# Kernel optimization log

Measured on AMD Instinct MI355X. Metric: run time of the kernel, lower is better.

Reference implementation:

```python
import jax, jax.numpy as jnp
import numpy as np

B, N, DIM, HEADS, DIM_HEAD = 2, 2048, 1024, 16, 64
INNER = HEADS * DIM_HEAD  # 1024
SCALE = DIM_HEAD ** -0.5
EPS = 1e-5  # fp32 path in the source


def _layernorm_seq(x, g):
    # Faithful to the repo's LayerNorm: statistics over dim=1 (sequence axis),
    # unbiased=False variance, clamp(min=eps).rsqrt(), scale by g over last axis.
    mean = jnp.mean(x, axis=1, keepdims=True)            # [b,1,d]
    var = jnp.mean((x - mean) ** 2, axis=1, keepdims=True)
    return (x - mean) * jax.lax.rsqrt(jnp.maximum(var, EPS)) * g


def setup_inputs() -> dict:
    key = jax.random.key(0)
    ks = jax.random.split(key, 5)
    x = jax.random.normal(ks[0], (B, N, DIM), dtype=jnp.float32)
    rel_pos_bias = jax.random.normal(ks[1], (1, HEADS, N, N), dtype=jnp.float32)
    g = jnp.ones((DIM,), dtype=jnp.float32)
    wq = jax.random.normal(ks[2], (INNER, DIM), dtype=jnp.float32) * (DIM ** -0.5)
    wkv = jax.random.normal(ks[3], (2 * INNER, DIM), dtype=jnp.float32) * (DIM ** -0.5)
    wout = jax.random.normal(ks[4], (DIM, INNER), dtype=jnp.float32) * (INNER ** -0.5)
    return {"x": x, "rel_pos_bias": rel_pos_bias, "g": g, "wq": wq, "wkv": wkv, "wout": wout}


def reference(x, rel_pos_bias, g, wq, wkv, wout):
    # self-attention path: context = x, framerate = None
    xn = _layernorm_seq(x, g)           # [b,n,d]
    cn = xn                              # context is None -> same tensor, same norm
    q = jnp.einsum('bnd,ed->bne', xn, wq)        # [b,n,inner]
    kv = jnp.einsum('bnd,ed->bne', cn, wkv)      # [b,n,2*inner]
    k, v = jnp.split(kv, 2, axis=-1)
    def heads(t):
        return t.reshape(B, N, HEADS, DIM_HEAD).transpose(0, 2, 1, 3)  # b h n d
    q, k, v = heads(q) * SCALE, heads(k), heads(v)
    sim = jnp.einsum('bhid,bhjd->bhij', q, k) + rel_pos_bias
    attn = jax.nn.softmax(sim, axis=-1)
    out = jnp.einsum('bhij,bhjd->bhid', attn, v)
    out = out.transpose(0, 2, 1, 3).reshape(B, N, INNER)  # b n (h d)
    return jnp.einsum('bne,de->bnd', out, wout)
```

## Files before the change

### kernel.cpp

```cpp
#include <hip/hip_runtime.h>
#include <hip/hip_bf16.h>
#include <stdint.h>

#define B_ 2
#define N_ 2048
#define DIM_ 1024
#define HEADS_ 16
#define DH_ 64
#define EPS_ 1e-5f

typedef __attribute__((ext_vector_type(4))) float f32x4;
typedef __attribute__((ext_vector_type(8))) float f32x8;
typedef __attribute__((ext_vector_type(16))) float f32x16;
typedef __attribute__((ext_vector_type(8))) __bf16 bf16x8;
typedef __attribute__((ext_vector_type(4))) unsigned int u32x4;
typedef __attribute__((ext_vector_type(2))) unsigned int u32x2;

__device__ __forceinline__ f32x4 mfma16(bf16x8 a, bf16x8 b, f32x4 c) {
  return __builtin_amdgcn_mfma_f32_16x16x32_bf16(a, b, c, 0, 0, 0);
}

__device__ __forceinline__ f32x16 mfma32(bf16x8 a, bf16x8 b, f32x16 c) {
  return __builtin_amdgcn_mfma_f32_32x32x16_bf16(a, b, c, 0, 0, 0);
}

__device__ __forceinline__ unsigned short f2bf(float x) {
  unsigned int u = __builtin_bit_cast(unsigned int, x);
  u += 0x7fffu + ((u >> 16) & 1u);
  return (unsigned short)(u >> 16);
}

__device__ __forceinline__ unsigned int cvt_pk_bf16(float lo, float hi) {
  unsigned int r;
  asm("v_cvt_pk_bf16_f32 %0, %1, %2" : "=v"(r) : "v"(lo), "v"(hi));
  return r;
}

__device__ __forceinline__ float uasf(unsigned int u) { return __builtin_bit_cast(float, u); }
__device__ __forceinline__ unsigned int fasu(float f) { return __builtin_bit_cast(unsigned int, f); }

__device__ __forceinline__ bf16x8 ld_frag(const unsigned short* p) {
  u32x4 v = *reinterpret_cast<const u32x4*>(p);
  return __builtin_bit_cast(bf16x8, v);
}

__device__ __forceinline__ void gload_lds16(const unsigned short* g, unsigned short* l) {
  __builtin_amdgcn_global_load_lds((const __attribute__((address_space(1))) void*)g,
                                   (__attribute__((address_space(3))) void*)l, 16, 0, 0);
}

__global__ __launch_bounds__(256) void ln_part(const float* __restrict__ x,
                                               float* __restrict__ ps,
                                               float* __restrict__ pss) {
  const int d = blockIdx.x * 256 + threadIdx.x;
  const int b = blockIdx.y >> 4, sp = blockIdx.y & 15;
  const float* xp = x + (size_t)(b * N_ + sp * 128) * DIM_ + d;
  float s = 0.f, ss = 0.f;
  for (int i = 0; i < 128; ++i) {
    float v = xp[(size_t)i * DIM_];
    s += v;
    ss += v * v;
  }
  int c = b * DIM_ + d;
  ps[sp * (B_ * DIM_) + c] = s;
  pss[sp * (B_ * DIM_) + c] = ss;
}

__global__ void ln_fin(const float* __restrict__ ps, const float* __restrict__ pss,
                       const float* __restrict__ g, float* __restrict__ meanA,
                       float* __restrict__ sclA) {
  int c = blockIdx.x * 256 + threadIdx.x;
  float s = 0.f, ss = 0.f;
#pragma unroll
  for (int sp = 0; sp < 16; ++sp) {
    s += ps[sp * (B_ * DIM_) + c];
    ss += pss[sp * (B_ * DIM_) + c];
  }
  float m = s * (1.f / N_);
  float v = ss * (1.f / N_) - m * m;
  meanA[c] = m;
  sclA[c] = rsqrtf(fmaxf(v, EPS_)) * g[c & (DIM_ - 1)];
}

__global__ __launch_bounds__(256) void ln_apply(const float* __restrict__ x,
                                                const float* __restrict__ meanA,
                                                const float* __restrict__ sclA,
                                                unsigned short* __restrict__ xn) {
  size_t t = (size_t)blockIdx.x * 256 + threadIdx.x;
  size_t base = t * 8;
  int d0 = (int)(base & (DIM_ - 1));
  int b = base >= (size_t)N_ * DIM_;
  int c = b * DIM_ + d0;
  const float4* xp = reinterpret_cast<const float4*>(x + base);
  const float4* mp = reinterpret_cast<const float4*>(meanA + c);
  const float4* sp = reinterpret_cast<const float4*>(sclA + c);
  float4 x0 = xp[0], x1 = xp[1];
  float4 m0 = mp[0], m1 = mp[1];
  float4 s0 = sp[0], s1 = sp[1];
  union {
    unsigned short u[8];
    u32x4 v;
  } o;
  o.u[0] = f2bf((x0.x - m0.x) * s0.x);
  o.u[1] = f2bf((x0.y - m0.y) * s0.y);
  o.u[2] = f2bf((x0.z - m0.z) * s0.z);
  o.u[3] = f2bf((x0.w - m0.w) * s0.w);
  o.u[4] = f2bf((x1.x - m1.x) * s1.x);
  o.u[5] = f2bf((x1.y - m1.y) * s1.y);
  o.u[6] = f2bf((x1.z - m1.z) * s1.z);
  o.u[7] = f2bf((x1.w - m1.w) * s1.w);
  *reinterpret_cast<u32x4*>(xn + base) = o.v;
}

__global__ __launch_bounds__(256) void cast_bf16(const float* __restrict__ src,
                                                 unsigned short* __restrict__ dst, float scale) {
  size_t t = (size_t)blockIdx.x * 256 + threadIdx.x;
  size_t base = t * 8;
  const float4* sp = reinterpret_cast<const float4*>(src + base);
  float4 a = sp[0], b4 = sp[1];
  union {
    unsigned short u[8];
    u32x4 v;
  } o;
  o.u[0] = f2bf(a.x * scale);
  o.u[1] = f2bf(a.y * scale);
  o.u[2] = f2bf(a.z * scale);
  o.u[3] = f2bf(a.w * scale);
  o.u[4] = f2bf(b4.x * scale);
  o.u[5] = f2bf(b4.y * scale);
  o.u[6] = f2bf(b4.z * scale);
  o.u[7] = f2bf(b4.w * scale);
  *reinterpret_cast<u32x4*>(dst + base) = o.v;
}

template <bool OUT_F32>
__global__ __launch_bounds__(256) void gemm_bt(const unsigned short* __restrict__ A,
                                               const unsigned short* __restrict__ W,
                                               void* __restrict__ Cout, int K, int ldc) {
  __shared__ unsigned short sA[128 * 64];
  __shared__ unsigned short sB[128 * 64];
  const int tid = threadIdx.x, lane = tid & 63, w = tid >> 6;
  const int wm = w >> 1, wn = w & 1;
  const int l15 = lane & 15, l4 = lane >> 4;
  const int m0 = blockIdx.y * 128, n0 = blockIdx.x * 128;
  f32x4 acc[4][4] = {};
  for (int kt = 0; kt < K; kt += 64) {
    __syncthreads();
#pragma unroll
    for (int p = 0; p < 4; ++p) {
      int flat = p * 256 + tid;
      int row = flat >> 3, c = flat & 7;
      int cs = c ^ (row & 7);
      gload_lds16(A + (size_t)(m0 + row) * K + kt + cs * 8, sA + (size_t)(p * 256 + w * 64) * 8);
      gload_lds16(W + (size_t)(n0 + row) * K + kt + cs * 8, sB + (size_t)(p * 256 + w * 64) * 8);
    }
    __syncthreads();
#pragma unroll
    for (int kk = 0; kk < 2; ++kk) {
      bf16x8 af[4], bfr[4];
#pragma unroll
      for (int i = 0; i < 4; ++i) {
        int rowA = wm * 64 + i * 16 + l15;
        af[i] = ld_frag(sA + rowA * 64 + (((kk * 4 + l4) ^ (rowA & 7)) * 8));
        int rowB = wn * 64 + i * 16 + l15;
        bfr[i] = ld_frag(sB + rowB * 64 + (((kk * 4 + l4) ^ (rowB & 7)) * 8));
      }
#pragma unroll
      for (int i = 0; i < 4; ++i)
#pragma unroll
        for (int j = 0; j < 4; ++j) acc[i][j] = mfma16(af[i], bfr[j], acc[i][j]);
    }
  }
#pragma unroll
  for (int i = 0; i < 4; ++i)
#pragma unroll
    for (int j = 0; j < 4; ++j)
#pragma unroll
      for (int r = 0; r < 4; ++r) {
        size_t off =
            (size_t)(m0 + wm * 64 + i * 16 + l4 * 4 + r) * ldc + (n0 + wn * 64 + j * 16 + l15);
        if (OUT_F32)
          ((float*)Cout)[off] = acc[i][j][r];
        else
          ((unsigned short*)Cout)[off] = f2bf(acc[i][j][r]);
      }
}

__global__ __launch_bounds__(256) void transpose_v(const unsigned short* __restrict__ qkv,
                                                   unsigned short* __restrict__ Vt) {
  __shared__ unsigned short tt[64][65];
  const int tid = threadIdx.x;
  const int h = blockIdx.y >> 1, b = blockIdx.y & 1;
  const int n0 = blockIdx.x * 64;
  const unsigned short* src = qkv + (size_t)(b * N_ + n0) * 3072 + 2048 + h * 64;
#pragma unroll
  for (int i = 0; i < 16; ++i) {
    int idx = i * 256 + tid;
    int r = idx >> 6, c = idx & 63;
    tt[r][c] = src[(size_t)r * 3072 + c];
  }
  __syncthreads();
  unsigned short* dst = Vt + (size_t)(b * HEADS_ + h) * 64 * N_ + n0;
#pragma unroll
  for (int i = 0; i < 16; ++i) {
    int idx = i * 256 + tid;
    int dh = idx >> 6, nn = idx & 63;
    dst[(size_t)dh * N_ + nn] = tt[nn][dh];
  }
}

__global__ __launch_bounds__(512, 2) void flash_attn(const unsigned short* __restrict__ qkv,
                                                     const float* __restrict__ bias,
                                                     const unsigned short* __restrict__ Vt,
                                                     unsigned short* __restrict__ Oatt) {
  __shared__ unsigned short sK[128 * 64];
  __shared__ unsigned short sV[64 * 128];
  __shared__ float sBias[8][32 * 128];

  const int tid = threadIdx.x, lane = tid & 63, w = tid >> 6;
  const int l31 = lane & 31, hi = lane >> 5;
  const int r = blockIdx.x;
  const int bh = r & 31, iblk = r >> 5;
  const int h = bh & 15, b = bh >> 4;
  const int qbase = iblk * 256 + w * 32;

  const unsigned short* Kg = qkv + (size_t)b * N_ * 3072 + 1024 + h * 64;
  const unsigned short* VtB = Vt + (size_t)(b * HEADS_ + h) * 64 * N_;
  const float* bias_h = bias + (size_t)h * N_ * N_;

  const int kflat0 = tid, kflat1 = 512 + tid;
  const int krow0 = kflat0 >> 3, kc0 = (kflat0 & 7) ^ (krow0 & 7);
  const int krow1 = kflat1 >> 3, kc1 = (kflat1 & 7) ^ (krow1 & 7);
  const int vrow0 = kflat0 >> 4, vc0 = (kflat0 & 15) ^ (vrow0 & 15);
  const int vrow1 = kflat1 >> 4, vc1 = (kflat1 & 15) ^ (vrow1 & 15);
  unsigned short* sKb0 = sK + (size_t)(w * 64) * 8;
  unsigned short* sKb1 = sK + (size_t)(512 + w * 64) * 8;
  unsigned short* sVb0 = sV + (size_t)(w * 64) * 8;
  unsigned short* sVb1 = sV + (size_t)(512 + w * 64) * 8;

#define STAGE_KV(JN)                                                       \
  gload_lds16(Kg + (size_t)((JN) + krow0) * 3072 + kc0 * 8, sKb0);         \
  gload_lds16(Kg + (size_t)((JN) + krow1) * 3072 + kc1 * 8, sKb1);         \
  gload_lds16(VtB + (size_t)vrow0 * N_ + (JN) + vc0 * 8, sVb0);            \
  gload_lds16(VtB + (size_t)vrow1 * N_ + (JN) + vc1 * 8, sVb1);

  float* sBw = sBias[w];
  unsigned short* sBw_us = reinterpret_cast<unsigned short*>(sBw);
  const int brr = lane >> 5, bsl = lane & 31;
  const float* bQ = bias_h + (size_t)qbase * N_;
#define SBI(i, JN)                                                            \
  gload_lds16((const unsigned short*)(bQ + (size_t)(2 * (i) + brr) * N_ +     \
                                      (JN) + ((bsl ^ (2 * (i) + brr)) << 2)), \
              sBw_us + (i) * 512);
#define STAGE_BIAS(JN)                                                     \
  SBI(0, JN) SBI(1, JN) SBI(2, JN) SBI(3, JN) SBI(4, JN) SBI(5, JN)        \
  SBI(6, JN) SBI(7, JN) SBI(8, JN) SBI(9, JN) SBI(10, JN) SBI(11, JN)      \
  SBI(12, JN) SBI(13, JN) SBI(14, JN) SBI(15, JN)

#define LDBIAS(DST, CB)                                                        \
  {                                                                            \
    const float* myB_ = sBw + l31 * 128;                                       \
    f32x4 t0 = *reinterpret_cast<const f32x4*>(myB_ + ((((CB) + 0 + hi) ^ l31) << 2)); \
    f32x4 t1 = *reinterpret_cast<const f32x4*>(myB_ + ((((CB) + 2 + hi) ^ l31) << 2)); \
    f32x4 t2 = *reinterpret_cast<const f32x4*>(myB_ + ((((CB) + 4 + hi) ^ l31) << 2)); \
    f32x4 t3 = *reinterpret_cast<const f32x4*>(myB_ + ((((CB) + 6 + hi) ^ l31) << 2)); \
    f32x8 u0_ = __builtin_shufflevector(t0, t1, 0, 1, 2, 3, 4, 5, 6, 7);       \
    f32x8 u1_ = __builtin_shufflevector(t2, t3, 0, 1, 2, 3, 4, 5, 6, 7);       \
    DST = __builtin_shufflevector(u0_, u1_, 0, 1, 2, 3, 4, 5, 6, 7, 8, 9, 10,  \
                                  11, 12, 13, 14, 15);                         \
  }

#define FRAGK(OUT, ROWB, CH)                                              \
  {                                                                       \
    int row_ = (ROWB) + l31;                                              \
    OUT = ld_frag(sK + row_ * 64 + (((CH) ^ (row_ & 7)) * 8));            \
  }
#define FRAGV(OUT, ROWB, CH)                                              \
  {                                                                       \
    int row_ = (ROWB) + l31;                                              \
    OUT = ld_frag(sV + row_ * 128 + (((CH) ^ (row_ & 15)) * 8));          \
  }

#define PACK2(S, PLO, PHI)                                                 \
  {                                                                        \
    unsigned int w0 = cvt_pk_bf16(S[0], S[1]), w1 = cvt_pk_bf16(S[2], S[3]);     \
    unsigned int w2 = cvt_pk_bf16(S[4], S[5]), w3 = cvt_pk_bf16(S[6], S[7]);     \
    unsigned int w4 = cvt_pk_bf16(S[8], S[9]), w5 = cvt_pk_bf16(S[10], S[11]);   \
    unsigned int w6 = cvt_pk_bf16(S[12], S[13]), w7 = cvt_pk_bf16(S[14], S[15]); \
    auto rA = __builtin_amdgcn_permlane32_swap(w0, w2, false, false);      \
    auto rB = __builtin_amdgcn_permlane32_swap(w1, w3, false, false);      \
    auto rC = __builtin_amdgcn_permlane32_swap(w4, w6, false, false);      \
    auto rD = __builtin_amdgcn_permlane32_swap(w5, w7, false, false);      \
    u32x4 pw;                                                              \
    pw[0] = rA[0]; pw[1] = rB[0]; pw[2] = rA[1]; pw[3] = rB[1];            \
    PLO = __builtin_bit_cast(bf16x8, pw);                                  \
    pw[0] = rC[0]; pw[1] = rD[0]; pw[2] = rC[1]; pw[3] = rD[1];            \
    PHI = __builtin_bit_cast(bf16x8, pw);                                  \
  }

  bf16x8 qf0, qf1, qf2, qf3;
  {
    const unsigned short* Qg =
        qkv + (size_t)(b * N_ + qbase + l31) * 3072 + h * 64 + hi * 8;
    qf0 = ld_frag(Qg);
    qf1 = ld_frag(Qg + 16);
    qf2 = ld_frag(Qg + 32);
    qf3 = ld_frag(Qg + 48);
  }

  f32x16 o0 = {}, o1 = {};
  float m_run = -1e30f, l_run = 0.f;

  STAGE_KV(0)
  STAGE_BIAS(0)

  const int NP = N_ / 128;
  for (int p = 0; p < NP; ++p) {
    asm volatile("s_waitcnt vmcnt(0) lgkmcnt(0)" ::: "memory");
    __builtin_amdgcn_s_barrier();

    f32x16 SA0, SA1, SB0, SB1;
    LDBIAS(SA0, 0)
    LDBIAS(SA1, 8)
    LDBIAS(SB0, 16)
    LDBIAS(SB1, 24)
    asm volatile("s_waitcnt lgkmcnt(0)" ::: "memory");
    __builtin_amdgcn_sched_barrier(0);

    if (p + 1 < NP) {
      const size_t jn = (size_t)(p + 1) * 128;
      STAGE_BIAS(jn)
    }

    __builtin_amdgcn_s_setprio(1);
    {
      bf16x8 kf;
      FRAGK(kf, 0, 0 + hi)  SA0 = mfma32(kf, qf0, SA0);
      FRAGK(kf, 0, 2 + hi)  SA0 = mfma32(kf, qf1, SA0);
      FRAGK(kf, 0, 4 + hi)  SA0 = mfma32(kf, qf2, SA0);
      FRAGK(kf, 0, 6 + hi)  SA0 = mfma32(kf, qf3, SA0);
      FRAGK(kf, 32, 0 + hi) SA1 = mfma32(kf, qf0, SA1);
      FRAGK(kf, 32, 2 + hi) SA1 = mfma32(kf, qf1, SA1);
      FRAGK(kf, 32, 4 + hi) SA1 = mfma32(kf, qf2, SA1);
      FRAGK(kf, 32, 6 + hi) SA1 = mfma32(kf, qf3, SA1);
      FRAGK(kf, 64, 0 + hi) SB0 = mfma32(kf, qf0, SB0);
      FRAGK(kf, 64, 2 + hi) SB0 = mfma32(kf, qf1, SB0);
      FRAGK(kf, 64, 4 + hi) SB0 = mfma32(kf, qf2, SB0);
      FRAGK(kf, 64, 6 + hi) SB0 = mfma32(kf, qf3, SB0);
      FRAGK(kf, 96, 0 + hi) SB1 = mfma32(kf, qf0, SB1);
      FRAGK(kf, 96, 2 + hi) SB1 = mfma32(kf, qf1, SB1);
      FRAGK(kf, 96, 4 + hi) SB1 = mfma32(kf, qf2, SB1);
      FRAGK(kf, 96, 6 + hi) SB1 = mfma32(kf, qf3, SB1);
    }
    __builtin_amdgcn_s_setprio(0);

    float c0 = SA0[0], c1 = SA1[0], c2 = SB0[0], c3 = SB1[0];
#pragma unroll
    for (int i = 1; i < 16; ++i) {
      c0 = fmaxf(c0, SA0[i]);
      c1 = fmaxf(c1, SA1[i]);
      c2 = fmaxf(c2, SB0[i]);
      c3 = fmaxf(c3, SB1[i]);
    }
    float mx = fmaxf(fmaxf(c0, c1), fmaxf(c2, c3));
    {
      auto pr_ = __builtin_amdgcn_permlane32_swap(fasu(mx), fasu(mx), false, false);
      mx = fmaxf(uasf(pr_[0]), uasf(pr_[1]));
    }
    float mn = fmaxf(m_run, mx);
    float alpha = __expf(m_run - mn);
#pragma unroll
    for (int i = 0; i < 16; ++i) {
      SA0[i] = __expf(SA0[i] - mn);
      SA1[i] = __expf(SA1[i] - mn);
      SB0[i] = __expf(SB0[i] - mn);
      SB1[i] = __expf(SB1[i] - mn);
    }
    float r0 = 0.f, r1 = 0.f, r2 = 0.f, r3 = 0.f;
#pragma unroll
    for (int i = 0; i < 16; ++i) {
      r0 += SA0[i];
      r1 += SA1[i];
      r2 += SB0[i];
      r3 += SB1[i];
    }
    float rs = (r0 + r1) + (r2 + r3);
    {
      auto pr_ = __builtin_amdgcn_permlane32_swap(fasu(rs), fasu(rs), false, false);
      rs = uasf(pr_[0]) + uasf(pr_[1]);
    }
    l_run = l_run * alpha + rs;
    m_run = mn;
#pragma unroll
    for (int i = 0; i < 16; ++i) {
      o0[i] *= alpha;
      o1[i] *= alpha;
    }

    bf16x8 pA0, pA1, pA2, pA3, pB0, pB1, pB2, pB3;
    PACK2(SA0, pA0, pA1)
    PACK2(SA1, pA2, pA3)
    PACK2(SB0, pB0, pB1)
    PACK2(SB1, pB2, pB3)

    __builtin_amdgcn_s_setprio(1);
    {
      bf16x8 vf;
      FRAGV(vf, 0, 0 + hi)   o0 = mfma32(vf, pA0, o0);
      FRAGV(vf, 0, 2 + hi)   o0 = mfma32(vf, pA1, o0);
      FRAGV(vf, 0, 4 + hi)   o0 = mfma32(vf, pA2, o0);
      FRAGV(vf, 0, 6 + hi)   o0 = mfma32(vf, pA3, o0);
      FRAGV(vf, 0, 8 + hi)   o0 = mfma32(vf, pB0, o0);
      FRAGV(vf, 0, 10 + hi)  o0 = mfma32(vf, pB1, o0);
      FRAGV(vf, 0, 12 + hi)  o0 = mfma32(vf, pB2, o0);
      FRAGV(vf, 0, 14 + hi)  o0 = mfma32(vf, pB3, o0);
      FRAGV(vf, 32, 0 + hi)  o1 = mfma32(vf, pA0, o1);
      FRAGV(vf, 32, 2 + hi)  o1 = mfma32(vf, pA1, o1);
      FRAGV(vf, 32, 4 + hi)  o1 = mfma32(vf, pA2, o1);
      FRAGV(vf, 32, 6 + hi)  o1 = mfma32(vf, pA3, o1);
      FRAGV(vf, 32, 8 + hi)  o1 = mfma32(vf, pB0, o1);
      FRAGV(vf, 32, 10 + hi) o1 = mfma32(vf, pB1, o1);
      FRAGV(vf, 32, 12 + hi) o1 = mfma32(vf, pB2, o1);
      FRAGV(vf, 32, 14 + hi) o1 = mfma32(vf, pB3, o1);
    }
    __builtin_amdgcn_s_setprio(0);

    asm volatile("s_waitcnt lgkmcnt(0)" ::: "memory");
    __builtin_amdgcn_s_barrier();
    if (p + 1 < NP) {
      const size_t jn = (size_t)(p + 1) * 128;
      STAGE_KV(jn)
    }
  }
#undef STAGE_KV
#undef SBI
#undef STAGE_BIAS
#undef LDBIAS
#undef FRAGK
#undef FRAGV
#undef PACK2

  float inv = 1.f / l_run;
  unsigned short* orow =
      Oatt + (size_t)(b * N_ + qbase + l31) * 1024 + h * 64 + hi * 4;
#pragma unroll
  for (int g = 0; g < 4; ++g) {
    u32x2 pk0;
    pk0[0] = cvt_pk_bf16(o0[g * 4 + 0] * inv, o0[g * 4 + 1] * inv);
    pk0[1] = cvt_pk_bf16(o0[g * 4 + 2] * inv, o0[g * 4 + 3] * inv);
    *reinterpret_cast<u32x2*>(orow + g * 8) = pk0;
    u32x2 pk1;
    pk1[0] = cvt_pk_bf16(o1[g * 4 + 0] * inv, o1[g * 4 + 1] * inv);
    pk1[1] = cvt_pk_bf16(o1[g * 4 + 2] * inv, o1[g * 4 + 3] * inv);
    *reinterpret_cast<u32x2*>(orow + 32 + g * 8) = pk1;
  }
}

extern "C" void kernel_launch(void* const* d_in, const int* in_sizes, int n_in, void* d_out,
                              int out_size, void* d_ws, size_t ws_size, hipStream_t stream) {
  const float* x = (const float*)d_in[0];
  const float* bias = (const float*)d_in[1];
  const float* g = (const float*)d_in[2];
  const float* wq = (const float*)d_in[3];
  const float* wkv = (const float*)d_in[4];
  const float* wout = (const float*)d_in[5];
  float* out = (float*)d_out;

  float* ps = (float*)d_ws;
  float* pss = ps + 16 * B_ * DIM_;
  float* meanA = pss + 16 * B_ * DIM_;
  float* sclA = meanA + B_ * DIM_;
  unsigned short* xn = (unsigned short*)(sclA + B_ * DIM_);
  unsigned short* Wqkv = xn + (size_t)4096 * 1024;
  unsigned short* WoutB = Wqkv + (size_t)3072 * 1024;
  unsigned short* qkvb = WoutB + (size_t)1024 * 1024;
  unsigned short* Vt = qkvb + (size_t)4096 * 3072;
  unsigned short* Oatt = xn;

  ln_part<<<dim3(DIM_ / 256, B_ * 16), 256, 0, stream>>>(x, ps, pss);
  ln_fin<<<dim3((B_ * DIM_) / 256), 256, 0, stream>>>(ps, pss, g, meanA, sclA);
  ln_apply<<<dim3((B_ * N_ * DIM_) / 2048), 256, 0, stream>>>(x, meanA, sclA, xn);
  cast_bf16<<<dim3((DIM_ * DIM_) / 2048), 256, 0, stream>>>(wq, Wqkv, 0.125f);
  cast_bf16<<<dim3((2 * DIM_ * DIM_) / 2048), 256, 0, stream>>>(wkv, Wqkv + (size_t)DIM_ * DIM_,
                                                                1.0f);
  cast_bf16<<<dim3((DIM_ * DIM_) / 2048), 256, 0, stream>>>(wout, WoutB, 1.0f);
  gemm_bt<false><<<dim3(3072 / 128, 4096 / 128), 256, 0, stream>>>(xn, Wqkv, qkvb, DIM_, 3072);
  transpose_v<<<dim3(N_ / 64, B_ * HEADS_), 256, 0, stream>>>(qkvb, Vt);
  flash_attn<<<dim3(256), 512, 0, stream>>>(qkvb, bias, Vt, Oatt);
  gemm_bt<true><<<dim3(1024 / 128, 4096 / 128), 256, 0, stream>>>(Oatt, WoutB, out, DIM_, 1024);
}
```

Baseline: 173.8 us.

## Double-buffer K/V and bias tiles with 64-key steps in flash attention

Shrinks the key tile from 128 to 64 and double-buffers the K, V and bias shared-memory tiles. Loads for the next K/V tile and the bias tile two steps ahead are issued while the current tile is computed, with a partial vmcnt wait in place of a full drain. This also removes the second barrier per iteration. In exchange the loop runs twice as many iterations, each with its own softmax rescale and barrier, and the swizzle and wait-count logic is more intricate.

```diff
diff --git a/kernel.cpp b/kernel.cpp
--- a/kernel.cpp
+++ b/kernel.cpp
@@ -213,72 +213,67 @@
                                                      const float* __restrict__ bias,
                                                      const unsigned short* __restrict__ Vt,
                                                      unsigned short* __restrict__ Oatt) {
-  __shared__ unsigned short sK[128 * 64];
-  __shared__ unsigned short sV[64 * 128];
-  __shared__ float sBias[8][32 * 128];
+  __shared__ unsigned short sK[2][64 * 64];
+  __shared__ unsigned short sV[2][64 * 64];
+  __shared__ float sBias[8][2][32 * 64];
 
   const int tid = threadIdx.x, lane = tid & 63, w = tid >> 6;
   const int l31 = lane & 31, hi = lane >> 5;
   const int r = blockIdx.x;
   const int bh = r & 31, iblk = r >> 5;
   const int h = bh & 15, b = bh >> 4;
-  const int qbase = iblk * 256 + w * 32;
+  const int qwb = iblk * 256 + w * 32;
 
   const unsigned short* Kg = qkv + (size_t)b * N_ * 3072 + 1024 + h * 64;
   const unsigned short* VtB = Vt + (size_t)(b * HEADS_ + h) * 64 * N_;
   const float* bias_h = bias + (size_t)h * N_ * N_;
 
-  const int kflat0 = tid, kflat1 = 512 + tid;
-  const int krow0 = kflat0 >> 3, kc0 = (kflat0 & 7) ^ (krow0 & 7);
-  const int krow1 = kflat1 >> 3, kc1 = (kflat1 & 7) ^ (krow1 & 7);
-  const int vrow0 = kflat0 >> 4, vc0 = (kflat0 & 15) ^ (vrow0 & 15);
-  const int vrow1 = kflat1 >> 4, vc1 = (kflat1 & 15) ^ (vrow1 & 15);
-  unsigned short* sKb0 = sK + (size_t)(w * 64) * 8;
-  unsigned short* sKb1 = sK + (size_t)(512 + w * 64) * 8;
-  unsigned short* sVb0 = sV + (size_t)(w * 64) * 8;
-  unsigned short* sVb1 = sV + (size_t)(512 + w * 64) * 8;
-
-#define STAGE_KV(JN)                                                       \
-  gload_lds16(Kg + (size_t)((JN) + krow0) * 3072 + kc0 * 8, sKb0);         \
-  gload_lds16(Kg + (size_t)((JN) + krow1) * 3072 + kc1 * 8, sKb1);         \
-  gload_lds16(VtB + (size_t)vrow0 * N_ + (JN) + vc0 * 8, sVb0);            \
-  gload_lds16(VtB + (size_t)vrow1 * N_ + (JN) + vc1 * 8, sVb1);
-
-  float* sBw = sBias[w];
-  unsigned short* sBw_us = reinterpret_cast<unsigned short*>(sBw);
-  const int brr = lane >> 5, bsl = lane & 31;
-  const float* bQ = bias_h + (size_t)qbase * N_;
-#define SBI(i, JN)                                                            \
-  gload_lds16((const unsigned short*)(bQ + (size_t)(2 * (i) + brr) * N_ +     \
-                                      (JN) + ((bsl ^ (2 * (i) + brr)) << 2)), \
-              sBw_us + (i) * 512);
-#define STAGE_BIAS(JN)                                                     \
-  SBI(0, JN) SBI(1, JN) SBI(2, JN) SBI(3, JN) SBI(4, JN) SBI(5, JN)        \
-  SBI(6, JN) SBI(7, JN) SBI(8, JN) SBI(9, JN) SBI(10, JN) SBI(11, JN)      \
-  SBI(12, JN) SBI(13, JN) SBI(14, JN) SBI(15, JN)
-
-#define LDBIAS(DST, CB)                                                        \
+  const int krow = w * 8 + (lane >> 3);
+  const int kcs = (lane & 7) ^ (krow & 7);
+  const unsigned short* kSrc = Kg + (size_t)krow * 3072 + kcs * 8;
+  const unsigned short* vSrc = VtB + (size_t)krow * N_ + kcs * 8;
+
+#define STAGE_KV(S, JN)                                      \
+  gload_lds16(kSrc + (size_t)(JN) * 3072, sK[S] + w * 512);  \
+  gload_lds16(vSrc + (JN), sV[S] + w * 512);
+
+  const int ln4b = lane >> 4, l15b = lane & 15;
+  const float* bp0 =
+      bias_h + (size_t)(qwb + 0 + ln4b) * N_ + ((l15b ^ ((0 + ln4b) & 15)) << 2);
+  const float* bp1 =
+      bias_h + (size_t)(qwb + 4 + ln4b) * N_ + ((l15b ^ ((4 + ln4b) & 15)) << 2);
+  const float* bp2 =
+      bias_h + (size_t)(qwb + 8 + ln4b) * N_ + ((l15b ^ ((8 + ln4b) & 15)) << 2);
+  const float* bp3 =
+      bias_h + (size_t)(qwb + 12 + ln4b) * N_ + ((l15b ^ ((12 + ln4b) & 15)) << 2);
+
+#define STAGE_BIAS(DSTUS, JN)                                                  \
+  gload_lds16((const unsigned short*)(bp0 + (JN)), (DSTUS) + 0 * 512);         \
+  gload_lds16((const unsigned short*)(bp1 + (JN)), (DSTUS) + 1 * 512);         \
+  gload_lds16((const unsigned short*)(bp2 + (JN)), (DSTUS) + 2 * 512);         \
+  gload_lds16((const unsigned short*)(bp3 + (JN)), (DSTUS) + 3 * 512);         \
+  gload_lds16((const unsigned short*)(bp0 + 16 * N_ + (JN)), (DSTUS) + 4 * 512); \
+  gload_lds16((const unsigned short*)(bp1 + 16 * N_ + (JN)), (DSTUS) + 5 * 512); \
+  gload_lds16((const unsigned short*)(bp2 + 16 * N_ + (JN)), (DSTUS) + 6 * 512); \
+  gload_lds16((const unsigned short*)(bp3 + 16 * N_ + (JN)), (DSTUS) + 7 * 512);
+
+#define LDBIAS(DST, MYB, CHB)                                                  \
   {                                                                            \
-    const float* myB_ = sBw + l31 * 128;                                       \
-    f32x4 t0 = *reinterpret_cast<const f32x4*>(myB_ + ((((CB) + 0 + hi) ^ l31) << 2)); \
-    f32x4 t1 = *reinterpret_cast<const f32x4*>(myB_ + ((((CB) + 2 + hi) ^ l31) << 2)); \
-    f32x4 t2 = *reinterpret_cast<const f32x4*>(myB_ + ((((CB) + 4 + hi) ^ l31) << 2)); \
-    f32x4 t3 = *reinterpret_cast<const f32x4*>(myB_ + ((((CB) + 6 + hi) ^ l31) << 2)); \
+    const float* myB_ = (MYB) + (size_t)l31 * 64;                              \
+    f32x4 t0 = *reinterpret_cast<const f32x4*>(myB_ + ((((CHB) + 0 + hi) ^ (l31 & 15)) << 2)); \
+    f32x4 t1 = *reinterpret_cast<const f32x4*>(myB_ + ((((CHB) + 2 + hi) ^ (l31 & 15)) << 2)); \
+    f32x4 t2 = *reinterpret_cast<const f32x4*>(myB_ + ((((CHB) + 4 + hi) ^ (l31 & 15)) << 2)); \
+    f32x4 t3 = *reinterpret_cast<const f32x4*>(myB_ + ((((CHB) + 6 + hi) ^ (l31 & 15)) << 2)); \
     f32x8 u0_ = __builtin_shufflevector(t0, t1, 0, 1, 2, 3, 4, 5, 6, 7);       \
     f32x8 u1_ = __builtin_shufflevector(t2, t3, 0, 1, 2, 3, 4, 5, 6, 7);       \
     DST = __builtin_shufflevector(u0_, u1_, 0, 1, 2, 3, 4, 5, 6, 7, 8, 9, 10,  \
                                   11, 12, 13, 14, 15);                         \
   }
 
-#define FRAGK(OUT, ROWB, CH)                                              \
-  {                                                                       \
-    int row_ = (ROWB) + l31;                                              \
-    OUT = ld_frag(sK + row_ * 64 + (((CH) ^ (row_ & 7)) * 8));            \
-  }
-#define FRAGV(OUT, ROWB, CH)                                              \
-  {                                                                       \
-    int row_ = (ROWB) + l31;                                              \
-    OUT = ld_frag(sV + row_ * 128 + (((CH) ^ (row_ & 15)) * 8));          \
+#define FRAGK(OUT, SRC, ROWB, CH)                                       \
+  {                                                                     \
+    int row_ = (ROWB) + l31;                                            \
+    OUT = ld_frag((SRC) + row_ * 64 + (((CH) ^ (row_ & 7)) * 8));       \
   }
 
 #define PACK2(S, PLO, PHI)                                                 \
@@ -301,7 +296,7 @@
   bf16x8 qf0, qf1, qf2, qf3;
   {
     const unsigned short* Qg =
-        qkv + (size_t)(b * N_ + qbase + l31) * 3072 + h * 64 + hi * 8;
+        qkv + (size_t)(b * N_ + qwb + l31) * 3072 + h * 64 + hi * 8;
     qf0 = ld_frag(Qg);
     qf1 = ld_frag(Qg + 16);
     qf2 = ld_frag(Qg + 32);
@@ -311,58 +306,62 @@
   f32x16 o0 = {}, o1 = {};
   float m_run = -1e30f, l_run = 0.f;
 
-  STAGE_KV(0)
-  STAGE_BIAS(0)
-
-  const int NP = N_ / 128;
-  for (int p = 0; p < NP; ++p) {
-    asm volatile("s_waitcnt vmcnt(0) lgkmcnt(0)" ::: "memory");
+  STAGE_BIAS(reinterpret_cast<unsigned short*>(&sBias[w][0][0]), 0)
+  __builtin_amdgcn_sched_barrier(0);
+  STAGE_KV(0, 0)
+  __builtin_amdgcn_sched_barrier(0);
+  STAGE_BIAS(reinterpret_cast<unsigned short*>(&sBias[w][1][0]), 64)
+  __builtin_amdgcn_sched_barrier(0);
+
+  const int NT = N_ / 64;
+  for (int j = 0; j < NT; ++j) {
+    if (j == NT - 1)
+      asm volatile("s_waitcnt vmcnt(0)" ::: "memory");
+    else
+      asm volatile("s_waitcnt vmcnt(8)" ::: "memory");
     __builtin_amdgcn_s_barrier();
-
-    f32x16 SA0, SA1, SB0, SB1;
-    LDBIAS(SA0, 0)
-    LDBIAS(SA1, 8)
-    LDBIAS(SB0, 16)
-    LDBIAS(SB1, 24)
+    const int slot = j & 1;
+    const unsigned short* sKc = sK[slot];
+    const unsigned short* sVc = sV[slot];
+    float* sBw = &sBias[w][slot][0];
+
+    if (j + 1 < NT) {
+      STAGE_KV(slot ^ 1, (size_t)(j + 1) * 64)
+      __builtin_amdgcn_sched_barrier(0);
+    }
+
+    f32x16 SA0, SA1;
+    LDBIAS(SA0, sBw, 0)
+    LDBIAS(SA1, sBw, 8)
     asm volatile("s_waitcnt lgkmcnt(0)" ::: "memory");
     __builtin_amdgcn_sched_barrier(0);
 
-    if (p + 1 < NP) {
-      const size_t jn = (size_t)(p + 1) * 128;
-      STAGE_BIAS(jn)
+    if (j + 2 < NT) {
+      STAGE_BIAS(reinterpret_cast<unsigned short*>(sBw), (size_t)(j + 2) * 64)
+      __builtin_amdgcn_sched_barrier(0);
     }
 
     __builtin_amdgcn_s_setprio(1);
     {
       bf16x8 kf;
-      FRAGK(kf, 0, 0 + hi)  SA0 = mfma32(kf, qf0, SA0);
-      FRAGK(kf, 0, 2 + hi)  SA0 = mfma32(kf, qf1, SA0);
-      FRAGK(kf, 0, 4 + hi)  SA0 = mfma32(kf, qf2, SA0);
-      FRAGK(kf, 0, 6 + hi)  SA0 = mfma32(kf, qf3, SA0);
-      FRAGK(kf, 32, 0 + hi) SA1 = mfma32(kf, qf0, SA1);
-      FRAGK(kf, 32, 2 + hi) SA1 = mfma32(kf, qf1, SA1);
-      FRAGK(kf, 32, 4 + hi) SA1 = mfma32(kf, qf2, SA1);
-      FRAGK(kf, 32, 6 + hi) SA1 = mfma32(kf, qf3, SA1);
-      FRAGK(kf, 64, 0 + hi) SB0 = mfma32(kf, qf0, SB0);
-      FRAGK(kf, 64, 2 + hi) SB0 = mfma32(kf, qf1, SB0);
-      FRAGK(kf, 64, 4 + hi) SB0 = mfma32(kf, qf2, SB0);
-      FRAGK(kf, 64, 6 + hi) SB0 = mfma32(kf, qf3, SB0);
-      FRAGK(kf, 96, 0 + hi) SB1 = mfma32(kf, qf0, SB1);
-      FRAGK(kf, 96, 2 + hi) SB1 = mfma32(kf, qf1, SB1);
-      FRAGK(kf, 96, 4 + hi) SB1 = mfma32(kf, qf2, SB1);
-      FRAGK(kf, 96, 6 + hi) SB1 = mfma32(kf, qf3, SB1);
+      FRAGK(kf, sKc, 0, 0 + hi)  SA0 = mfma32(kf, qf0, SA0);
+      FRAGK(kf, sKc, 0, 2 + hi)  SA0 = mfma32(kf, qf1, SA0);
+      FRAGK(kf, sKc, 0, 4 + hi)  SA0 = mfma32(kf, qf2, SA0);
+      FRAGK(kf, sKc, 0, 6 + hi)  SA0 = mfma32(kf, qf3, SA0);
+      FRAGK(kf, sKc, 32, 0 + hi) SA1 = mfma32(kf, qf0, SA1);
+      FRAGK(kf, sKc, 32, 2 + hi) SA1 = mfma32(kf, qf1, SA1);
+      FRAGK(kf, sKc, 32, 4 + hi) SA1 = mfma32(kf, qf2, SA1);
+      FRAGK(kf, sKc, 32, 6 + hi) SA1 = mfma32(kf, qf3, SA1);
     }
     __builtin_amdgcn_s_setprio(0);
 
-    float c0 = SA0[0], c1 = SA1[0], c2 = SB0[0], c3 = SB1[0];
+    float c0 = SA0[0], c1 = SA1[0];
 #pragma unroll
     for (int i = 1; i < 16; ++i) {
       c0 = fmaxf(c0, SA0[i]);
       c1 = fmaxf(c1, SA1[i]);
-      c2 = fmaxf(c2, SB0[i]);
-      c3 = fmaxf(c3, SB1[i]);
-    }
-    float mx = fmaxf(fmaxf(c0, c1), fmaxf(c2, c3));
+    }
+    float mx = fmaxf(c0, c1);
     {
       auto pr_ = __builtin_amdgcn_permlane32_swap(fasu(mx), fasu(mx), false, false);
       mx = fmaxf(uasf(pr_[0]), uasf(pr_[1]));
@@ -373,18 +372,14 @@
     for (int i = 0; i < 16; ++i) {
       SA0[i] = __expf(SA0[i] - mn);
       SA1[i] = __expf(SA1[i] - mn);
-      SB0[i] = __expf(SB0[i] - mn);
-      SB1[i] = __expf(SB1[i] - mn);
-    }
-    float r0 = 0.f, r1 = 0.f, r2 = 0.f, r3 = 0.f;
+    }
+    float r0 = 0.f, r1 = 0.f;
 #pragma unroll
     for (int i = 0; i < 16; ++i) {
       r0 += SA0[i];
       r1 += SA1[i];
-      r2 += SB0[i];
-      r3 += SB1[i];
-    }
-    float rs = (r0 + r1) + (r2 + r3);
+    }
+    float rs = r0 + r1;
     {
       auto pr_ = __builtin_amdgcn_permlane32_swap(fasu(rs), fasu(rs), false, false);
       rs = uasf(pr_[0]) + uasf(pr_[1]);
@@ -397,52 +392,33 @@
       o1[i] *= alpha;
     }
 
-    bf16x8 pA0, pA1, pA2, pA3, pB0, pB1, pB2, pB3;
+    bf16x8 pA0, pA1, pA2, pA3;
     PACK2(SA0, pA0, pA1)
     PACK2(SA1, pA2, pA3)
-    PACK2(SB0, pB0, pB1)
-    PACK2(SB1, pB2, pB3)
 
     __builtin_amdgcn_s_setprio(1);
     {
       bf16x8 vf;
-      FRAGV(vf, 0, 0 + hi)   o0 = mfma32(vf, pA0, o0);
-      FRAGV(vf, 0, 2 + hi)   o0 = mfma32(vf, pA1, o0);
-      FRAGV(vf, 0, 4 + hi)   o0 = mfma32(vf, pA2, o0);
-      FRAGV(vf, 0, 6 + hi)   o0 = mfma32(vf, pA3, o0);
-      FRAGV(vf, 0, 8 + hi)   o0 = mfma32(vf, pB0, o0);
-      FRAGV(vf, 0, 10 + hi)  o0 = mfma32(vf, pB1, o0);
-      FRAGV(vf, 0, 12 + hi)  o0 = mfma32(vf, pB2, o0);
-      FRAGV(vf, 0, 14 + hi)  o0 = mfma32(vf, pB3, o0);
-      FRAGV(vf, 32, 0 + hi)  o1 = mfma32(vf, pA0, o1);
-      FRAGV(vf, 32, 2 + hi)  o1 = mfma32(vf, pA1, o1);
-      FRAGV(vf, 32, 4 + hi)  o1 = mfma32(vf, pA2, o1);
-      FRAGV(vf, 32, 6 + hi)  o1 = mfma32(vf, pA3, o1);
-      FRAGV(vf, 32, 8 + hi)  o1 = mfma32(vf, pB0, o1);
-      FRAGV(vf, 32, 10 + hi) o1 = mfma32(vf, pB1, o1);
-      FRAGV(vf, 32, 12 + hi) o1 = mfma32(vf, pB2, o1);
-      FRAGV(vf, 32, 14 + hi) o1 = mfma32(vf, pB3, o1);
+      FRAGK(vf, sVc, 0, 0 + hi)  o0 = mfma32(vf, pA0, o0);
+      FRAGK(vf, sVc, 0, 2 + hi)  o0 = mfma32(vf, pA1, o0);
+      FRAGK(vf, sVc, 0, 4 + hi)  o0 = mfma32(vf, pA2, o0);
+      FRAGK(vf, sVc, 0, 6 + hi)  o0 = mfma32(vf, pA3, o0);
+      FRAGK(vf, sVc, 32, 0 + hi) o1 = mfma32(vf, pA0, o1);
+      FRAGK(vf, sVc, 32, 2 + hi) o1 = mfma32(vf, pA1, o1);
+      FRAGK(vf, sVc, 32, 4 + hi) o1 = mfma32(vf, pA2, o1);
+      FRAGK(vf, sVc, 32, 6 + hi) o1 = mfma32(vf, pA3, o1);
     }
     __builtin_amdgcn_s_setprio(0);
-
-    asm volatile("s_waitcnt lgkmcnt(0)" ::: "memory");
-    __builtin_amdgcn_s_barrier();
-    if (p + 1 < NP) {
-      const size_t jn = (size_t)(p + 1) * 128;
-      STAGE_KV(jn)
-    }
   }
 #undef STAGE_KV
-#undef SBI
 #undef STAGE_BIAS
 #undef LDBIAS
 #undef FRAGK
-#undef FRAGV
 #undef PACK2
 
   float inv = 1.f / l_run;
   unsigned short* orow =
-      Oatt + (size_t)(b * N_ + qbase + l31) * 1024 + h * 64 + hi * 4;
+      Oatt + (size_t)(b * N_ + qwb + l31) * 1024 + h * 64 + hi * 4;
 #pragma unroll
   for (int g = 0; g < 4; ++g) {
     u32x2 pk0;
```

Result: slower. 189.3 us (+8.9%).

## Share relative-position bias tiles across both batches in flash attention blocks

Applied to the files above, without the earlier changes.

Each workgroup now covers one head and 128 query rows for both batch elements. Waves 0-3 take batch 0 and waves 4-7 take batch 1 over the same query rows, so the bias tile (which has no batch dimension) is loaded into LDS once and used by both halves. This halves global bias traffic, which is the dominant stream here. In exchange, K/V LDS buffers double to hold both batches, every wave stages part of the shared bias, and an extra barrier is added after reading bias so it is not overwritten by the next prefetch.

```diff
diff --git a/kernel.cpp b/kernel.cpp
--- a/kernel.cpp
+++ b/kernel.cpp
@@ -213,53 +213,89 @@
                                                      const float* __restrict__ bias,
                                                      const unsigned short* __restrict__ Vt,
                                                      unsigned short* __restrict__ Oatt) {
-  __shared__ unsigned short sK[128 * 64];
-  __shared__ unsigned short sV[64 * 128];
-  __shared__ float sBias[8][32 * 128];
+  __shared__ unsigned short sK[2 * 128 * 64];
+  __shared__ unsigned short sV[2 * 64 * 128];
+  __shared__ float sBias[4][32 * 128];
 
   const int tid = threadIdx.x, lane = tid & 63, w = tid >> 6;
   const int l31 = lane & 31, hi = lane >> 5;
-  const int r = blockIdx.x;
-  const int bh = r & 31, iblk = r >> 5;
-  const int h = bh & 15, b = bh >> 4;
-  const int qbase = iblk * 256 + w * 32;
-
-  const unsigned short* Kg = qkv + (size_t)b * N_ * 3072 + 1024 + h * 64;
-  const unsigned short* VtB = Vt + (size_t)(b * HEADS_ + h) * 64 * N_;
+  const int id = blockIdx.x;
+  const int h = id & 15, iblk = id >> 4;
+  const int sl = w & 3, wb = w >> 2;
+  const int qwb = iblk * 128 + sl * 32;
+
+  const unsigned short* Kg0 = qkv + 1024 + h * 64;
+  const unsigned short* Kg1 = Kg0 + (size_t)N_ * 3072;
+  const unsigned short* Vt0 = Vt + (size_t)h * 64 * N_;
+  const unsigned short* Vt1 = Vt0 + (size_t)HEADS_ * 64 * N_;
   const float* bias_h = bias + (size_t)h * N_ * N_;
 
-  const int kflat0 = tid, kflat1 = 512 + tid;
-  const int krow0 = kflat0 >> 3, kc0 = (kflat0 & 7) ^ (krow0 & 7);
-  const int krow1 = kflat1 >> 3, kc1 = (kflat1 & 7) ^ (krow1 & 7);
-  const int vrow0 = kflat0 >> 4, vc0 = (kflat0 & 15) ^ (vrow0 & 15);
-  const int vrow1 = kflat1 >> 4, vc1 = (kflat1 & 15) ^ (vrow1 & 15);
-  unsigned short* sKb0 = sK + (size_t)(w * 64) * 8;
-  unsigned short* sKb1 = sK + (size_t)(512 + w * 64) * 8;
-  unsigned short* sVb0 = sV + (size_t)(w * 64) * 8;
-  unsigned short* sVb1 = sV + (size_t)(512 + w * 64) * 8;
-
-#define STAGE_KV(JN)                                                       \
-  gload_lds16(Kg + (size_t)((JN) + krow0) * 3072 + kc0 * 8, sKb0);         \
-  gload_lds16(Kg + (size_t)((JN) + krow1) * 3072 + kc1 * 8, sKb1);         \
-  gload_lds16(VtB + (size_t)vrow0 * N_ + (JN) + vc0 * 8, sVb0);            \
-  gload_lds16(VtB + (size_t)vrow1 * N_ + (JN) + vc1 * 8, sVb1);
-
-  float* sBw = sBias[w];
-  unsigned short* sBw_us = reinterpret_cast<unsigned short*>(sBw);
+  const int krow_t = tid >> 3, kcs_t = (tid & 7) ^ (krow_t & 7);
+  const unsigned short* kS0 = Kg0 + (size_t)krow_t * 3072 + kcs_t * 8;
+  const unsigned short* kS1 = kS0 + (size_t)64 * 3072;
+  const unsigned short* kS2 = Kg1 + (size_t)krow_t * 3072 + kcs_t * 8;
+  const unsigned short* kS3 = kS2 + (size_t)64 * 3072;
+  unsigned short* kD0 = sK + (size_t)(0 * 512 + w * 64) * 8;
+  unsigned short* kD1 = sK + (size_t)(1 * 512 + w * 64) * 8;
+  unsigned short* kD2 = sK + (size_t)(2 * 512 + w * 64) * 8;
+  unsigned short* kD3 = sK + (size_t)(3 * 512 + w * 64) * 8;
+
+  const int vrow_t = tid >> 4, vcs_t = (tid & 15) ^ (vrow_t & 15);
+  const unsigned short* vS0 = Vt0 + (size_t)vrow_t * N_ + vcs_t * 8;
+  const unsigned short* vS1 = vS0 + (size_t)32 * N_;
+  const unsigned short* vS2 = Vt1 + (size_t)vrow_t * N_ + vcs_t * 8;
+  const unsigned short* vS3 = vS2 + (size_t)32 * N_;
+  unsigned short* vD0 = sV + (size_t)(0 * 512 + w * 64) * 8;
+  unsigned short* vD1 = sV + (size_t)(1 * 512 + w * 64) * 8;
+  unsigned short* vD2 = sV + (size_t)(2 * 512 + w * 64) * 8;
+  unsigned short* vD3 = sV + (size_t)(3 * 512 + w * 64) * 8;
+
+#define STAGE_KV(JN)                                  \
+  gload_lds16(kS0 + (size_t)(JN) * 3072, kD0);        \
+  gload_lds16(kS1 + (size_t)(JN) * 3072, kD1);        \
+  gload_lds16(kS2 + (size_t)(JN) * 3072, kD2);        \
+  gload_lds16(kS3 + (size_t)(JN) * 3072, kD3);        \
+  gload_lds16(vS0 + (JN), vD0);                       \
+  gload_lds16(vS1 + (JN), vD1);                       \
+  gload_lds16(vS2 + (JN), vD2);                       \
+  gload_lds16(vS3 + (JN), vD3);
+
   const int brr = lane >> 5, bsl = lane & 31;
-  const float* bQ = bias_h + (size_t)qbase * N_;
-#define SBI(i, JN)                                                            \
-  gload_lds16((const unsigned short*)(bQ + (size_t)(2 * (i) + brr) * N_ +     \
-                                      (JN) + ((bsl ^ (2 * (i) + brr)) << 2)), \
-              sBw_us + (i) * 512);
-#define STAGE_BIAS(JN)                                                     \
-  SBI(0, JN) SBI(1, JN) SBI(2, JN) SBI(3, JN) SBI(4, JN) SBI(5, JN)        \
-  SBI(6, JN) SBI(7, JN) SBI(8, JN) SBI(9, JN) SBI(10, JN) SBI(11, JN)      \
-  SBI(12, JN) SBI(13, JN) SBI(14, JN) SBI(15, JN)
+  const int rl0 = 16 * wb + 0 + brr, rl1 = 16 * wb + 2 + brr;
+  const int rl2 = 16 * wb + 4 + brr, rl3 = 16 * wb + 6 + brr;
+  const int rl4 = 16 * wb + 8 + brr, rl5 = 16 * wb + 10 + brr;
+  const int rl6 = 16 * wb + 12 + brr, rl7 = 16 * wb + 14 + brr;
+  const float* bq0 = bias_h + (size_t)(qwb + rl0) * N_ + ((bsl ^ rl0) << 2);
+  const float* bq1 = bias_h + (size_t)(qwb + rl1) * N_ + ((bsl ^ rl1) << 2);
+  const float* bq2 = bias_h + (size_t)(qwb + rl2) * N_ + ((bsl ^ rl2) << 2);
+  const float* bq3 = bias_h + (size_t)(qwb + rl3) * N_ + ((bsl ^ rl3) << 2);
+  const float* bq4 = bias_h + (size_t)(qwb + rl4) * N_ + ((bsl ^ rl4) << 2);
+  const float* bq5 = bias_h + (size_t)(qwb + rl5) * N_ + ((bsl ^ rl5) << 2);
+  const float* bq6 = bias_h + (size_t)(qwb + rl6) * N_ + ((bsl ^ rl6) << 2);
+  const float* bq7 = bias_h + (size_t)(qwb + rl7) * N_ + ((bsl ^ rl7) << 2);
+  unsigned short* sB_us = reinterpret_cast<unsigned short*>(sBias[sl]);
+  unsigned short* bD0 = sB_us + (size_t)(16 * wb + 0) * 256;
+  unsigned short* bD1 = sB_us + (size_t)(16 * wb + 2) * 256;
+  unsigned short* bD2 = sB_us + (size_t)(16 * wb + 4) * 256;
+  unsigned short* bD3 = sB_us + (size_t)(16 * wb + 6) * 256;
+  unsigned short* bD4 = sB_us + (size_t)(16 * wb + 8) * 256;
+  unsigned short* bD5 = sB_us + (size_t)(16 * wb + 10) * 256;
+  unsigned short* bD6 = sB_us + (size_t)(16 * wb + 12) * 256;
+  unsigned short* bD7 = sB_us + (size_t)(16 * wb + 14) * 256;
+
+#define STAGE_BIAS(JN)                                        \
+  gload_lds16((const unsigned short*)(bq0 + (JN)), bD0);      \
+  gload_lds16((const unsigned short*)(bq1 + (JN)), bD1);      \
+  gload_lds16((const unsigned short*)(bq2 + (JN)), bD2);      \
+  gload_lds16((const unsigned short*)(bq3 + (JN)), bD3);      \
+  gload_lds16((const unsigned short*)(bq4 + (JN)), bD4);      \
+  gload_lds16((const unsigned short*)(bq5 + (JN)), bD5);      \
+  gload_lds16((const unsigned short*)(bq6 + (JN)), bD6);      \
+  gload_lds16((const unsigned short*)(bq7 + (JN)), bD7);
 
 #define LDBIAS(DST, CB)                                                        \
   {                                                                            \
-    const float* myB_ = sBw + l31 * 128;                                       \
+    const float* myB_ = sBias[sl] + (size_t)l31 * 128;                         \
     f32x4 t0 = *reinterpret_cast<const f32x4*>(myB_ + ((((CB) + 0 + hi) ^ l31) << 2)); \
     f32x4 t1 = *reinterpret_cast<const f32x4*>(myB_ + ((((CB) + 2 + hi) ^ l31) << 2)); \
     f32x4 t2 = *reinterpret_cast<const f32x4*>(myB_ + ((((CB) + 4 + hi) ^ l31) << 2)); \
@@ -270,15 +306,18 @@
                                   11, 12, 13, 14, 15);                         \
   }
 
-#define FRAGK(OUT, ROWB, CH)                                              \
-  {                                                                       \
-    int row_ = (ROWB) + l31;                                              \
-    OUT = ld_frag(sK + row_ * 64 + (((CH) ^ (row_ & 7)) * 8));            \
-  }
-#define FRAGV(OUT, ROWB, CH)                                              \
-  {                                                                       \
-    int row_ = (ROWB) + l31;                                              \
-    OUT = ld_frag(sV + row_ * 128 + (((CH) ^ (row_ & 15)) * 8));          \
+  const unsigned short* sKb = sK + (size_t)wb * 128 * 64;
+  const unsigned short* sVb = sV + (size_t)wb * 64 * 128;
+
+#define FRAGK(OUT, ROWB, CH)                                            \
+  {                                                                     \
+    int row_ = (ROWB) + l31;                                            \
+    OUT = ld_frag(sKb + row_ * 64 + (((CH) ^ (row_ & 7)) * 8));         \
+  }
+#define FRAGV(OUT, ROWB, CH)                                            \
+  {                                                                     \
+    int row_ = (ROWB) + l31;                                            \
+    OUT = ld_frag(sVb + row_ * 128 + (((CH) ^ (row_ & 15)) * 8));       \
   }
 
 #define PACK2(S, PLO, PHI)                                                 \
@@ -301,7 +340,7 @@
   bf16x8 qf0, qf1, qf2, qf3;
   {
     const unsigned short* Qg =
-        qkv + (size_t)(b * N_ + qbase + l31) * 3072 + h * 64 + hi * 8;
+        qkv + (size_t)(wb * N_ + qwb + l31) * 3072 + h * 64 + hi * 8;
     qf0 = ld_frag(Qg);
     qf1 = ld_frag(Qg + 16);
     qf2 = ld_frag(Qg + 32);
@@ -326,6 +365,7 @@
     LDBIAS(SB1, 24)
     asm volatile("s_waitcnt lgkmcnt(0)" ::: "memory");
     __builtin_amdgcn_sched_barrier(0);
+    __builtin_amdgcn_s_barrier();
 
     if (p + 1 < NP) {
       const size_t jn = (size_t)(p + 1) * 128;
@@ -433,7 +473,6 @@
     }
   }
 #undef STAGE_KV
-#undef SBI
 #undef STAGE_BIAS
 #undef LDBIAS
 #undef FRAGK
@@ -442,7 +481,7 @@
 
   float inv = 1.f / l_run;
   unsigned short* orow =
-      Oatt + (size_t)(b * N_ + qbase + l31) * 1024 + h * 64 + hi * 4;
+      Oatt + (size_t)(wb * N_ + qwb + l31) * 1024 + h * 64 + hi * 4;
 #pragma unroll
   for (int g = 0; g < 4; ++g) {
     u32x2 pk0;
```

New measurement: 174.4 us. Within noise of the previous version (+0.4%).

## Double-buffer bias tiles and shrink attention blocks to four waves

Applied to the files above, without the earlier changes.

The flash attention kernel now runs 512 blocks of 256 threads (4 waves, 128 query rows) instead of 256 blocks of 512 threads. The bias tile in LDS is double-buffered per wave, so the next tile's bias loads are issued before the current tile's compute and waited on with a partial vmcnt instead of a full drain. The goal is to hide the large fp32 bias stream behind the MFMA work and to spread work over more blocks. In exchange, LDS per block grows, K/V tiles are reloaded by twice as many blocks, and occupancy is limited by launch bounds of one block.

```diff
diff --git a/kernel.cpp b/kernel.cpp
--- a/kernel.cpp
+++ b/kernel.cpp
@@ -209,57 +209,57 @@
   }
 }
 
-__global__ __launch_bounds__(512, 2) void flash_attn(const unsigned short* __restrict__ qkv,
+__global__ __launch_bounds__(256, 1) void flash_attn(const unsigned short* __restrict__ qkv,
                                                      const float* __restrict__ bias,
                                                      const unsigned short* __restrict__ Vt,
                                                      unsigned short* __restrict__ Oatt) {
   __shared__ unsigned short sK[128 * 64];
   __shared__ unsigned short sV[64 * 128];
-  __shared__ float sBias[8][32 * 128];
+  __shared__ float sBias[4][2][32 * 128];
 
   const int tid = threadIdx.x, lane = tid & 63, w = tid >> 6;
   const int l31 = lane & 31, hi = lane >> 5;
-  const int r = blockIdx.x;
-  const int bh = r & 31, iblk = r >> 5;
+  const int id = blockIdx.x;
+  const int bh = id & 31, iblk = id >> 5;
   const int h = bh & 15, b = bh >> 4;
-  const int qbase = iblk * 256 + w * 32;
+  const int qwb = iblk * 128 + w * 32;
 
   const unsigned short* Kg = qkv + (size_t)b * N_ * 3072 + 1024 + h * 64;
   const unsigned short* VtB = Vt + (size_t)(b * HEADS_ + h) * 64 * N_;
   const float* bias_h = bias + (size_t)h * N_ * N_;
 
-  const int kflat0 = tid, kflat1 = 512 + tid;
-  const int krow0 = kflat0 >> 3, kc0 = (kflat0 & 7) ^ (krow0 & 7);
-  const int krow1 = kflat1 >> 3, kc1 = (kflat1 & 7) ^ (krow1 & 7);
-  const int vrow0 = kflat0 >> 4, vc0 = (kflat0 & 15) ^ (vrow0 & 15);
-  const int vrow1 = kflat1 >> 4, vc1 = (kflat1 & 15) ^ (vrow1 & 15);
-  unsigned short* sKb0 = sK + (size_t)(w * 64) * 8;
-  unsigned short* sKb1 = sK + (size_t)(512 + w * 64) * 8;
-  unsigned short* sVb0 = sV + (size_t)(w * 64) * 8;
-  unsigned short* sVb1 = sV + (size_t)(512 + w * 64) * 8;
-
-#define STAGE_KV(JN)                                                       \
-  gload_lds16(Kg + (size_t)((JN) + krow0) * 3072 + kc0 * 8, sKb0);         \
-  gload_lds16(Kg + (size_t)((JN) + krow1) * 3072 + kc1 * 8, sKb1);         \
-  gload_lds16(VtB + (size_t)vrow0 * N_ + (JN) + vc0 * 8, sVb0);            \
-  gload_lds16(VtB + (size_t)vrow1 * N_ + (JN) + vc1 * 8, sVb1);
-
-  float* sBw = sBias[w];
-  unsigned short* sBw_us = reinterpret_cast<unsigned short*>(sBw);
+  const int kr = w * 8 + (lane >> 3);
+  const int kcs = (lane & 7) ^ (kr & 7);
+  const unsigned short* kSrc = Kg + (size_t)kr * 3072 + kcs * 8;
+  unsigned short* kDst = sK + (size_t)(w * 64) * 8;
+  const int vr = w * 4 + (lane >> 4);
+  const int vcs = (lane & 15) ^ (vr & 15);
+  const unsigned short* vSrc = VtB + (size_t)vr * N_ + vcs * 8;
+  unsigned short* vDst = sV + (size_t)(w * 64) * 8;
+
+#define STAGE_KV(JN)                                                          \
+  {                                                                           \
+    _Pragma("unroll") for (int q = 0; q < 4; ++q)                             \
+        gload_lds16(kSrc + ((size_t)(JN) + q * 32) * 3072, kDst + q * 2048);  \
+    _Pragma("unroll") for (int q = 0; q < 4; ++q)                             \
+        gload_lds16(vSrc + (size_t)(q * 16) * N_ + (JN), vDst + q * 2048);    \
+  }
+
   const int brr = lane >> 5, bsl = lane & 31;
-  const float* bQ = bias_h + (size_t)qbase * N_;
-#define SBI(i, JN)                                                            \
-  gload_lds16((const unsigned short*)(bQ + (size_t)(2 * (i) + brr) * N_ +     \
-                                      (JN) + ((bsl ^ (2 * (i) + brr)) << 2)), \
-              sBw_us + (i) * 512);
-#define STAGE_BIAS(JN)                                                     \
-  SBI(0, JN) SBI(1, JN) SBI(2, JN) SBI(3, JN) SBI(4, JN) SBI(5, JN)        \
-  SBI(6, JN) SBI(7, JN) SBI(8, JN) SBI(9, JN) SBI(10, JN) SBI(11, JN)      \
-  SBI(12, JN) SBI(13, JN) SBI(14, JN) SBI(15, JN)
-
-#define LDBIAS(DST, CB)                                                        \
+#define STAGE_BIAS(SLOT, JN)                                                   \
   {                                                                            \
-    const float* myB_ = sBw + l31 * 128;                                       \
+    unsigned short* d_ = reinterpret_cast<unsigned short*>(&sBias[w][SLOT][0]); \
+    _Pragma("unroll") for (int i = 0; i < 16; ++i) {                           \
+      int rl_ = 2 * i + brr;                                                   \
+      const float* s_ =                                                        \
+          bias_h + (size_t)(qwb + rl_) * N_ + (JN) + ((bsl ^ rl_) << 2);       \
+      gload_lds16((const unsigned short*)s_, d_ + i * 512);                    \
+    }                                                                          \
+  }
+
+#define LDBIAS(DST, MYB, CB)                                                   \
+  {                                                                            \
+    const float* myB_ = (MYB) + (size_t)l31 * 128;                             \
     f32x4 t0 = *reinterpret_cast<const f32x4*>(myB_ + ((((CB) + 0 + hi) ^ l31) << 2)); \
     f32x4 t1 = *reinterpret_cast<const f32x4*>(myB_ + ((((CB) + 2 + hi) ^ l31) << 2)); \
     f32x4 t2 = *reinterpret_cast<const f32x4*>(myB_ + ((((CB) + 4 + hi) ^ l31) << 2)); \
@@ -270,15 +270,15 @@
                                   11, 12, 13, 14, 15);                         \
   }
 
-#define FRAGK(OUT, ROWB, CH)                                              \
-  {                                                                       \
-    int row_ = (ROWB) + l31;                                              \
-    OUT = ld_frag(sK + row_ * 64 + (((CH) ^ (row_ & 7)) * 8));            \
-  }
-#define FRAGV(OUT, ROWB, CH)                                              \
-  {                                                                       \
-    int row_ = (ROWB) + l31;                                              \
-    OUT = ld_frag(sV + row_ * 128 + (((CH) ^ (row_ & 15)) * 8));          \
+#define FRAGK(OUT, ROWB, CH)                                            \
+  {                                                                     \
+    int row_ = (ROWB) + l31;                                            \
+    OUT = ld_frag(sK + row_ * 64 + (((CH) ^ (row_ & 7)) * 8));          \
+  }
+#define FRAGV(OUT, ROWB, CH)                                            \
+  {                                                                     \
+    int row_ = (ROWB) + l31;                                            \
+    OUT = ld_frag(sV + row_ * 128 + (((CH) ^ (row_ & 15)) * 8));        \
   }
 
 #define PACK2(S, PLO, PHI)                                                 \
@@ -301,7 +301,7 @@
   bf16x8 qf0, qf1, qf2, qf3;
   {
     const unsigned short* Qg =
-        qkv + (size_t)(b * N_ + qbase + l31) * 3072 + h * 64 + hi * 8;
+        qkv + (size_t)(b * N_ + qwb + l31) * 3072 + h * 64 + hi * 8;
     qf0 = ld_frag(Qg);
     qf1 = ld_frag(Qg + 16);
     qf2 = ld_frag(Qg + 32);
@@ -311,26 +311,31 @@
   f32x16 o0 = {}, o1 = {};
   float m_run = -1e30f, l_run = 0.f;
 
+  STAGE_BIAS(0, 0)
+  __builtin_amdgcn_sched_barrier(0);
   STAGE_KV(0)
-  STAGE_BIAS(0)
+  __builtin_amdgcn_sched_barrier(0);
 
   const int NP = N_ / 128;
-  for (int p = 0; p < NP; ++p) {
-    asm volatile("s_waitcnt vmcnt(0) lgkmcnt(0)" ::: "memory");
+  for (int j = 0; j < NP; ++j) {
+    const int slot = j & 1;
+    if (j + 1 < NP) {
+      STAGE_BIAS(slot ^ 1, (size_t)(j + 1) * 128)
+      __builtin_amdgcn_sched_barrier(0);
+      asm volatile("s_waitcnt vmcnt(16)" ::: "memory");
+    } else {
+      asm volatile("s_waitcnt vmcnt(0)" ::: "memory");
+    }
     __builtin_amdgcn_s_barrier();
 
     f32x16 SA0, SA1, SB0, SB1;
-    LDBIAS(SA0, 0)
-    LDBIAS(SA1, 8)
-    LDBIAS(SB0, 16)
-    LDBIAS(SB1, 24)
+    float* sBw = &sBias[w][slot][0];
+    LDBIAS(SA0, sBw, 0)
+    LDBIAS(SA1, sBw, 8)
+    LDBIAS(SB0, sBw, 16)
+    LDBIAS(SB1, sBw, 24)
     asm volatile("s_waitcnt lgkmcnt(0)" ::: "memory");
     __builtin_amdgcn_sched_barrier(0);
-
-    if (p + 1 < NP) {
-      const size_t jn = (size_t)(p + 1) * 128;
-      STAGE_BIAS(jn)
-    }
 
     __builtin_amdgcn_s_setprio(1);
     {
@@ -427,13 +432,12 @@
 
     asm volatile("s_waitcnt lgkmcnt(0)" ::: "memory");
     __builtin_amdgcn_s_barrier();
-    if (p + 1 < NP) {
-      const size_t jn = (size_t)(p + 1) * 128;
-      STAGE_KV(jn)
+    if (j + 1 < NP) {
+      STAGE_KV((size_t)(j + 1) * 128)
+      __builtin_amdgcn_sched_barrier(0);
     }
   }
 #undef STAGE_KV
-#undef SBI
 #undef STAGE_BIAS
 #undef LDBIAS
 #undef FRAGK
@@ -442,7 +446,7 @@
 
   float inv = 1.f / l_run;
   unsigned short* orow =
-      Oatt + (size_t)(b * N_ + qbase + l31) * 1024 + h * 64 + hi * 4;
+      Oatt + (size_t)(b * N_ + qwb + l31) * 1024 + h * 64 + hi * 4;
 #pragma unroll
   for (int g = 0; g < 4; ++g) {
     u32x2 pk0;
@@ -486,6 +490,6 @@
   cast_bf16<<<dim3((DIM_ * DIM_) / 2048), 256, 0, stream>>>(wout, WoutB, 1.0f);
   gemm_bt<false><<<dim3(3072 / 128, 4096 / 128), 256, 0, stream>>>(xn, Wqkv, qkvb, DIM_, 3072);
   transpose_v<<<dim3(N_ / 64, B_ * HEADS_), 256, 0, stream>>>(qkvb, Vt);
-  flash_attn<<<dim3(256), 512, 0, stream>>>(qkvb, bias, Vt, Oatt);
+  flash_attn<<<dim3(512), 256, 0, stream>>>(qkvb, bias, Vt, Oatt);
   gemm_bt<true><<<dim3(1024 / 128, 4096 / 128), 256, 0, stream>>>(Oatt, WoutB, out, DIM_, 1024);
 }
```

Result: slower. 222.1 us (+27.8%).
